# Kernel optimization log

Hardware: AMD Instinct MI355X
Metric: run time of the kernel (lower is better)

Reference implementation:

```python
import jax, jax.numpy as jnp
import numpy as np

B, S, HID = 2, 2048, 1024
NUM_HEADS, HEAD_DIM = 16, 64
GRID_SIZE = 16                 # crop_size // patch_size
ROT_DIM = 2 * (HEAD_DIM // 3 // 2)  # = 20, per axial segment (d, h, w)


def setup_inputs() -> dict:
    key = jax.random.key(0)
    ks = jax.random.split(key, 9)
    sc = 1.0 / np.sqrt(HID)
    return {
        "hidden_states": jax.random.normal(ks[0], (B, S, HID), jnp.float32),
        "Wq": jax.random.normal(ks[1], (HID, HID), jnp.float32) * sc,
        "bq": jax.random.normal(ks[2], (HID,), jnp.float32) * 0.02,
        "Wk": jax.random.normal(ks[3], (HID, HID), jnp.float32) * sc,
        "bk": jax.random.normal(ks[4], (HID,), jnp.float32) * 0.02,
        "Wv": jax.random.normal(ks[5], (HID, HID), jnp.float32) * sc,
        "bv": jax.random.normal(ks[6], (HID,), jnp.float32) * 0.02,
        "Wo": jax.random.normal(ks[7], (HID, HID), jnp.float32) * sc,
        "bo": jax.random.normal(ks[8], (HID,), jnp.float32) * 0.02,
    }


def _rotate(x, pos):
    # x: [B, H, S, D], pos: [S] int. Matches torch rotate_queries_or_keys:
    # sin/cos are TILED (repeat) along the last dim, not interleaved.
    D = x.shape[-1]
    half = D // 2
    omega = 1.0 / (10000.0 ** (jnp.arange(half, dtype=x.dtype) / half))
    freq = pos.astype(x.dtype)[:, None] * omega           # [S, half]
    sin = jnp.tile(jnp.sin(freq), (1, 2))                 # [S, D]
    cos = jnp.tile(jnp.cos(freq), (1, 2))
    y = x.reshape(x.shape[:-1] + (half, 2))
    rot = jnp.stack((-y[..., 1], y[..., 0]), axis=-1).reshape(x.shape)
    return x * cos + rot * sin


def _apply_axial_rope(qk, frame_ids, height_ids, width_ids):
    d = ROT_DIM
    parts = [
        _rotate(qk[..., 0:d], frame_ids),
        _rotate(qk[..., d:2 * d], height_ids),
        _rotate(qk[..., 2 * d:3 * d], width_ids),
    ]
    if 3 * d < qk.shape[-1]:
        parts.append(qk[..., 3 * d:])  # un-rotated tail
    return jnp.concatenate(parts, axis=-1)


def reference(hidden_states, Wq, bq, Wk, bk, Wv, bv, Wo, bo):
    Bq, Sq, _ = hidden_states.shape

    def heads(x):  # [B,S,HID] -> [B,H,S,Dh]
        return x.reshape(Bq, Sq, NUM_HEADS, HEAD_DIM).transpose(0, 2, 1, 3)

    q = heads(hidden_states @ Wq + bq)
    k = heads(hidden_states @ Wk + bk)
    v = heads(hidden_states @ Wv + bv)

    # 3D axial position ids from flat token index
    ids = jnp.arange(Sq)
    tokens_per_frame = GRID_SIZE * GRID_SIZE
    frame_ids = ids // tokens_per_frame
    rem = ids - tokens_per_frame * frame_ids
    height_ids = rem // GRID_SIZE
    width_ids = rem - GRID_SIZE * height_ids

    k = _apply_axial_rope(k, frame_ids, height_ids, width_ids)
    q = _apply_axial_rope(q, frame_ids, height_ids, width_ids)

    scaling = HEAD_DIM ** -0.5
    scores = jnp.einsum("bhqd,bhkd->bhqk", q, k) * scaling
    probs = jax.nn.softmax(scores.astype(jnp.float32), axis=-1).astype(q.dtype)
    ctx = jnp.einsum("bhqk,bhkd->bhqd", probs, v)
    ctx = ctx.transpose(0, 2, 1, 3).reshape(Bq, Sq, HID)
    return ctx @ Wo + bo
```

## Files before the change

kernel.cpp:

```cpp
#include <hip/hip_runtime.h>
#include <hip/hip_bf16.h>

#define B_   2
#define S_   2048
#define HID_ 1024
#define NH_  16
#define HD_  64

typedef __hip_bfloat16 bf16;
typedef __attribute__((ext_vector_type(8))) short s8v;
typedef __attribute__((ext_vector_type(4))) short s4v;
typedef __attribute__((ext_vector_type(4))) float f4v;

#define QSCALE 0.18033688011112042f

__device__ __forceinline__ unsigned short f2b_rne(float x) {
    unsigned int u = __float_as_uint(x);
    u += 0x7fffu + ((u >> 16) & 1u);
    return (unsigned short)(u >> 16);
}

__device__ __forceinline__ void gload_lds16(const void* g, void* l) {
    __builtin_amdgcn_global_load_lds(
        (const __attribute__((address_space(1))) void*)g,
        (__attribute__((address_space(3))) void*)l, 16, 0, 0);
}

__device__ __forceinline__ s4v pack_p(float p0, float p1, float p2, float p3) {
    union { uint2 u; s4v s; } c;
    c.u.x = __builtin_amdgcn_perm(__float_as_uint(p1), __float_as_uint(p0), 0x07060302u);
    c.u.y = __builtin_amdgcn_perm(__float_as_uint(p3), __float_as_uint(p2), 0x07060302u);
    return c.s;
}

__global__ __launch_bounds__(256) void prep_kernel(
    const float* __restrict__ X,
    const float* __restrict__ W0, const float* __restrict__ W1,
    const float* __restrict__ W2, const float* __restrict__ W3,
    unsigned short* __restrict__ Xb,
    unsigned short* __restrict__ T0, unsigned short* __restrict__ T1,
    unsigned short* __restrict__ T2, unsigned short* __restrict__ T3)
{
    const int z = blockIdx.z;
    const int t = threadIdx.x;

    if (z >= 4) {
        const size_t base = ((size_t)(z - 4) * 256 + blockIdx.y * 16 + blockIdx.x) * 4096;
        #pragma unroll
        for (int p = 0; p < 4; ++p) {
            const size_t i = base + p * 1024 + t * 4;
            const float4 f = *reinterpret_cast<const float4*>(X + i);
            ushort4 u;
            u.x = f2b_rne(f.x); u.y = f2b_rne(f.y); u.z = f2b_rne(f.z); u.w = f2b_rne(f.w);
            *reinterpret_cast<ushort4*>(Xb + i) = u;
        }
        return;
    }

    const float* __restrict__ W = (z == 0) ? W0 : (z == 1) ? W1 : (z == 2) ? W2 : W3;
    unsigned short* __restrict__ T = (z == 0) ? T0 : (z == 1) ? T1 : (z == 2) ? T2 : T3;

    __shared__ float Tl[64][65];
    const int n0 = blockIdx.x * 64, k0 = blockIdx.y * 64;
    const int rr = t >> 4, c4 = (t & 15) * 4;

    #pragma unroll
    for (int i = 0; i < 4; ++i) {
        const int kr = i * 16 + rr;
        const float4 f = *reinterpret_cast<const float4*>(W + (size_t)(k0 + kr) * HID_ + n0 + c4);
        Tl[c4 + 0][kr] = f.x; Tl[c4 + 1][kr] = f.y;
        Tl[c4 + 2][kr] = f.z; Tl[c4 + 3][kr] = f.w;
    }
    __syncthreads();
    #pragma unroll
    for (int i = 0; i < 4; ++i) {
        const int nr = i * 16 + rr;
        ushort4 u;
        u.x = f2b_rne(Tl[nr][c4 + 0]); u.y = f2b_rne(Tl[nr][c4 + 1]);
        u.z = f2b_rne(Tl[nr][c4 + 2]); u.w = f2b_rne(Tl[nr][c4 + 3]);
        *reinterpret_cast<ushort4*>(T + (size_t)(n0 + nr) * HID_ + k0 + c4) = u;
    }
}

__device__ __forceinline__ void gemm_stage(
    const unsigned short* __restrict__ Ag, const unsigned short* __restrict__ Bg,
    unsigned short* As, unsigned short* Bs,
    int m0, int n0, int k0, int w, int srow, int lc8)
{
    #pragma unroll
    for (int it = 0; it < 4; ++it) {
        const int row = it * 32 + srow;
        const int sb = (it * 256 + w * 64) * 8;
        gload_lds16(Ag + (size_t)(m0 + row) * HID_ + k0 + lc8, As + sb);
        gload_lds16(Bg + (size_t)(n0 + row) * HID_ + k0 + lc8, Bs + sb);
    }
}

__device__ __forceinline__ void mfma_mainloop_db(
    const unsigned short* __restrict__ Ag, const unsigned short* __restrict__ Bg,
    unsigned short (*As)[128 * 64], unsigned short (*Bs)[128 * 64],
    int m0, int n0, int t, f4v acc[4][4])
{
    const int w = t >> 6, lane = t & 63;
    const int l15 = lane & 15, qd = lane >> 4;
    const int wm = (w & 1) * 64, wn = (w >> 1) * 64;
    const int srow = w * 8 + (lane >> 3);
    const int lc8  = (((lane & 7) ^ (lane >> 3)) * 8);

    gemm_stage(Ag, Bg, As[0], Bs[0], m0, n0, 0, w, srow, lc8);

    for (int kt = 0; kt < HID_ / 64; ++kt) {
        __builtin_amdgcn_s_waitcnt(0x0f70);
        __builtin_amdgcn_s_barrier();
        if (kt < HID_ / 64 - 1)
            gemm_stage(Ag, Bg, As[(kt + 1) & 1], Bs[(kt + 1) & 1],
                       m0, n0, (kt + 1) * 64, w, srow, lc8);

        const unsigned short* Acur = As[kt & 1];
        const unsigned short* Bcur = Bs[kt & 1];
        #pragma unroll
        for (int kc = 0; kc < 2; ++kc) {
            const int p = ((kc * 4 + qd) ^ (l15 & 7)) * 8;
            s8v af[4], bf[4];
            #pragma unroll
            for (int mt = 0; mt < 4; ++mt)
                af[mt] = *reinterpret_cast<const s8v*>(Acur + (wm + mt * 16 + l15) * 64 + p);
            #pragma unroll
            for (int nt = 0; nt < 4; ++nt)
                bf[nt] = *reinterpret_cast<const s8v*>(Bcur + (wn + nt * 16 + l15) * 64 + p);
            #pragma unroll
            for (int mt = 0; mt < 4; ++mt)
                #pragma unroll
                for (int nt = 0; nt < 4; ++nt)
                    acc[mt][nt] = __builtin_amdgcn_mfma_f32_16x16x32_bf16(
                        af[mt], bf[nt], acc[mt][nt], 0, 0, 0);
        }
    }
}

__global__ __launch_bounds__(256, 2) void gemm_qkv_kernel(
    const unsigned short* __restrict__ Xb, const unsigned short* __restrict__ Wt,
    const float* __restrict__ bq, const float* __restrict__ bk, const float* __restrict__ bv,
    unsigned short* __restrict__ Qb, unsigned short* __restrict__ Kb,
    unsigned short* __restrict__ Vt)
{
    const int n0g = blockIdx.x * 128;
    const int z   = n0g >> 10;
    const int n0  = n0g & 1023;
    const int m0  = blockIdx.y * 128;
    const float* __restrict__ bias = (z == 0) ? bq : (z == 1) ? bk : bv;

    const int t = threadIdx.x;
    const int w = t >> 6, lane = t & 63;
    const int l15 = lane & 15, qd = lane >> 4;
    const int wm = (w & 1) * 64, wn = (w >> 1) * 64;

    __shared__ unsigned short As[2][128 * 64];
    __shared__ unsigned short Bs[2][128 * 64];

    f4v acc[4][4];
    #pragma unroll
    for (int mt = 0; mt < 4; ++mt)
        #pragma unroll
        for (int nt = 0; nt < 4; ++nt) acc[mt][nt] = (f4v){0.f, 0.f, 0.f, 0.f};

    mfma_mainloop_db(Xb, Wt, As, Bs, m0, n0g, t, acc);

    const float osc = (z == 0) ? QSCALE : 1.f;

    #pragma unroll
    for (int nt = 0; nt < 4; ++nt) {
        const int col = n0 + wn + nt * 16 + l15;
        const int h = col >> 6, d = col & 63;
        const float bsc = bias[col];
        const int seg = d / 20;
        const int ds  = d - seg * 20;
        const float om   = __expf(-0.9210340372f * (float)(ds % 10));
        const float sign = (d & 1) ? 1.f : -1.f;

        #pragma unroll
        for (int mt = 0; mt < 4; ++mt) {
            const int mbase = m0 + wm + mt * 16 + qd * 4;
            const int b = mbase >> 11;
            const int sbase = mbase & 2047;
            if (z == 2) {
                ushort4 u;
                unsigned short* up = (unsigned short*)&u;
                #pragma unroll
                for (int r = 0; r < 4; ++r) up[r] = f2b_rne(acc[mt][nt][r] + bsc);
                *reinterpret_cast<ushort4*>(
                    Vt + ((size_t)(b * NH_ + h) * HD_ + d) * S_ + sbase) = u;
            } else {
                unsigned short* __restrict__ dst = (z == 0 ? Qb : Kb)
                    + ((size_t)(b * NH_ + h) * S_ + sbase) * HD_ + d;
                #pragma unroll
                for (int r = 0; r < 4; ++r) {
                    const int s = sbase + r;
                    float v = acc[mt][nt][r] + bsc;
                    const float xp = __shfl_xor(v, 1);
                    if (d < 60) {
                        const int rem = s & 255;
                        const float pos = (float)(seg == 0 ? (s >> 8)
                                               : (seg == 1 ? (rem >> 4) : (rem & 15)));
                        const float a = pos * om;
                        float sn, cs;
                        __sincosf(a, &sn, &cs);
                        v = v * cs + sign * xp * sn;
                    }
                    dst[(size_t)r * HD_] = f2b_rne(v * osc);
                }
            }
        }
    }
}

__global__ __launch_bounds__(256, 2) void gemm_out_kernel(
    const unsigned short* __restrict__ Cb, const unsigned short* __restrict__ Wot,
    const float* __restrict__ bo, float* __restrict__ out)
{
    const int n0 = blockIdx.x * 128, m0 = blockIdx.y * 128;
    const int t = threadIdx.x;
    const int w = t >> 6, lane = t & 63;
    const int l15 = lane & 15, qd = lane >> 4;
    const int wm = (w & 1) * 64, wn = (w >> 1) * 64;

    __shared__ unsigned short As[2][128 * 64];
    __shared__ unsigned short Bs[2][128 * 64];

    f4v acc[4][4];
    #pragma unroll
    for (int mt = 0; mt < 4; ++mt)
        #pragma unroll
        for (int nt = 0; nt < 4; ++nt) acc[mt][nt] = (f4v){0.f, 0.f, 0.f, 0.f};

    mfma_mainloop_db(Cb, Wot, As, Bs, m0, n0, t, acc);

    #pragma unroll
    for (int nt = 0; nt < 4; ++nt) {
        const int col = n0 + wn + nt * 16 + l15;
        const float bsc = bo[col];
        #pragma unroll
        for (int mt = 0; mt < 4; ++mt) {
            const int mbase = m0 + wm + mt * 16 + qd * 4;
            #pragma unroll
            for (int r = 0; r < 4; ++r)
                out[(size_t)(mbase + r) * HID_ + col] = acc[mt][nt][r] + bsc;
        }
    }
}

__global__ __launch_bounds__(256, 2) void attn_kernel(
    const bf16* __restrict__ Qb, const bf16* __restrict__ Kb,
    const bf16* __restrict__ Vt, unsigned short* __restrict__ Cb)
{
    const int q0 = blockIdx.x * 128;
    const int bh = blockIdx.y;
    const int b  = bh >> 4, h = bh & 15;
    const int t  = threadIdx.x;
    const int w  = t >> 6;
    const int lane = t & 63;
    const int l15 = lane & 15, qd = lane >> 4;

    __shared__ unsigned short Ks[2][128 * 64];
    __shared__ unsigned short Vs[2][64 * 128];

    s8v bq[2][2];
    #pragma unroll
    for (int g = 0; g < 2; ++g) {
        const bf16* Qrow = Qb + ((size_t)bh * S_ + q0 + w * 32 + g * 16 + l15) * HD_ + qd * 8;
        bq[g][0] = *reinterpret_cast<const s8v*>(Qrow);
        bq[g][1] = *reinterpret_cast<const s8v*>(Qrow + 32);
    }

    f4v oacc[2][4];
    f4v lones[2];
    #pragma unroll
    for (int g = 0; g < 2; ++g) {
        lones[g] = (f4v){0.f, 0.f, 0.f, 0.f};
        #pragma unroll
        for (int dt = 0; dt < 4; ++dt) oacc[g][dt] = (f4v){0.f, 0.f, 0.f, 0.f};
    }

    s4v vone;
    { union { uint2 u; s4v s; } c; c.u = make_uint2(0x3F803F80u, 0x3F803F80u); vone = c.s; }

    const bf16* __restrict__ Kg = Kb + (size_t)bh * S_ * HD_;
    const bf16* __restrict__ Vg = Vt + (size_t)bh * HD_ * S_;

    const int krow = lane >> 3;
    const int ksw  = ((lane & 7) ^ krow) * 8;
    const int vrow = lane >> 4;

    auto stage = [&](int tile, unsigned short* Kd, unsigned short* Vd) {
        const int k0 = tile * 128;
        #pragma unroll
        for (int it = 0; it < 4; ++it) {
            gload_lds16(Kg + (size_t)(k0 + w * 32 + it * 8 + krow) * HD_ + ksw,
                        Kd + (w * 32 + it * 8) * 64);
        }
        #pragma unroll
        for (int it = 0; it < 4; ++it) {
            const int r = w * 16 + it * 4 + vrow;
            const int sv = ((lane & 15) ^ (r & 15)) * 8;
            gload_lds16(Vg + (size_t)r * S_ + k0 + sv,
                        Vd + (w * 16 + it * 4) * 128);
        }
    };

    stage(0, Ks[0], Vs[0]);

    for (int tt = 0; tt < S_ / 128; ++tt) {
        __builtin_amdgcn_s_waitcnt(0x0f70);
        __builtin_amdgcn_s_barrier();
        if (tt < S_ / 128 - 1)
            stage(tt + 1, Ks[(tt + 1) & 1], Vs[(tt + 1) & 1]);

        const unsigned short* K_ = Ks[tt & 1];
        const unsigned short* V_ = Vs[tt & 1];

        #pragma unroll
        for (int nt = 0; nt < 8; ++nt) {
            const unsigned short* kr = K_ + (nt * 16 + l15) * 64;
            const s8v ak0 = *reinterpret_cast<const s8v*>(kr + ((qd ^ (l15 & 7)) * 8));
            const s8v ak1 = *reinterpret_cast<const s8v*>(kr + (((qd + 4) ^ (l15 & 7)) * 8));

            s4v bv[4];
            #pragma unroll
            for (int dt = 0; dt < 4; ++dt) {
                const int r = dt * 16 + l15;
                const int c = nt * 2 + (qd >> 1);
                bv[dt] = *reinterpret_cast<const s4v*>(
                    V_ + r * 128 + ((c ^ l15) & 15) * 8 + (qd & 1) * 4);
            }

            #pragma unroll
            for (int g = 0; g < 2; ++g) {
                f4v zz = (f4v){0.f, 0.f, 0.f, 0.f};
                zz = __builtin_amdgcn_mfma_f32_16x16x32_bf16(ak0, bq[g][0], zz, 0, 0, 0);
                zz = __builtin_amdgcn_mfma_f32_16x16x32_bf16(ak1, bq[g][1], zz, 0, 0, 0);
                const float p0 = __builtin_amdgcn_exp2f(zz[0]);
                const float p1 = __builtin_amdgcn_exp2f(zz[1]);
                const float p2 = __builtin_amdgcn_exp2f(zz[2]);
                const float p3 = __builtin_amdgcn_exp2f(zz[3]);
                const s4v pf = pack_p(p0, p1, p2, p3);
                #pragma unroll
                for (int dt = 0; dt < 4; ++dt)
                    oacc[g][dt] = __builtin_amdgcn_mfma_f32_16x16x16bf16_1k(
                        pf, bv[dt], oacc[g][dt], 0, 0, 0);
                lones[g] = __builtin_amdgcn_mfma_f32_16x16x16bf16_1k(
                    pf, vone, lones[g], 0, 0, 0);
            }
        }
    }

    #pragma unroll
    for (int g = 0; g < 2; ++g) {
        #pragma unroll
        for (int r = 0; r < 4; ++r) {
            const float inv = 1.0f / lones[g][r];
            const int s = q0 + w * 32 + g * 16 + qd * 4 + r;
            unsigned short* __restrict__ dst =
                Cb + ((size_t)(b * S_ + s)) * HID_ + h * HD_ + l15;
            #pragma unroll
            for (int dt = 0; dt < 4; ++dt)
                dst[dt * 16] = f2b_rne(oacc[g][dt][r] * inv);
        }
    }
}

extern "C" void kernel_launch(void* const* d_in, const int* in_sizes, int n_in,
                              void* d_out, int out_size, void* d_ws, size_t ws_size,
                              hipStream_t stream)
{
    const float* X  = (const float*)d_in[0];
    const float* Wq = (const float*)d_in[1];
    const float* bq = (const float*)d_in[2];
    const float* Wk = (const float*)d_in[3];
    const float* bk = (const float*)d_in[4];
    const float* Wv = (const float*)d_in[5];
    const float* bv = (const float*)d_in[6];
    const float* Wo = (const float*)d_in[7];
    const float* bo = (const float*)d_in[8];
    float* out = (float*)d_out;

    const size_t QKV = (size_t)B_ * NH_ * S_ * HD_;
    const size_t WSZ = (size_t)HID_ * HID_;
    unsigned short* Wot = (unsigned short*)d_ws;
    unsigned short* Xb  = Wot + WSZ;
    unsigned short* Wqt = Xb  + QKV;
    unsigned short* Wkt = Wqt + WSZ;
    unsigned short* Wvt = Wkt + WSZ;
    unsigned short* Qb  = Wvt + WSZ;
    unsigned short* Kb  = Qb + QKV;
    unsigned short* Vt  = Kb + QKV;
    unsigned short* Cb  = Vt + QKV;

    prep_kernel<<<dim3(16, 16, 8), 256, 0, stream>>>(
        X, Wq, Wk, Wv, Wo, Xb, Wqt, Wkt, Wvt, Wot);
    gemm_qkv_kernel<<<dim3(24, 32), 256, 0, stream>>>(
        Xb, Wqt, bq, bk, bv, Qb, Kb, Vt);
    attn_kernel<<<dim3(S_ / 128, B_ * NH_), 256, 0, stream>>>(
        (const bf16*)Qb, (const bf16*)Kb, (const bf16*)Vt, Cb);
    gemm_out_kernel<<<dim3(8, 32), 256, 0, stream>>>(Cb, Wot, bo, out);
}
```

Before: 190.5 us.

## Replace ones-MFMA row-sum with VALU accumulation and remap blocks per XCD

The softmax denominator was computed by an extra MFMA against a vector of ones. It is now accumulated with VALU adds on the bf16-rounded probabilities and reduced across lanes with shuffles at the end, which removes one of five MFMAs per inner step. Work-group indices are also remapped so that consecutive blocks landing on the same XCD share the same batch-head, so K/V tiles get reused in that XCD's L2. The cost is extra VALU work and shuffles, and the remap assumes round-robin dispatch across eight XCDs.

```diff
diff --git a/kernel.cpp b/kernel.cpp
--- a/kernel.cpp
+++ b/kernel.cpp
@@ -24,13 +24,6 @@
     __builtin_amdgcn_global_load_lds(
         (const __attribute__((address_space(1))) void*)g,
         (__attribute__((address_space(3))) void*)l, 16, 0, 0);
-}
-
-__device__ __forceinline__ s4v pack_p(float p0, float p1, float p2, float p3) {
-    union { uint2 u; s4v s; } c;
-    c.u.x = __builtin_amdgcn_perm(__float_as_uint(p1), __float_as_uint(p0), 0x07060302u);
-    c.u.y = __builtin_amdgcn_perm(__float_as_uint(p3), __float_as_uint(p2), 0x07060302u);
-    return c.s;
 }
 
 __global__ __launch_bounds__(256) void prep_kernel(
@@ -253,8 +246,11 @@
     const bf16* __restrict__ Qb, const bf16* __restrict__ Kb,
     const bf16* __restrict__ Vt, unsigned short* __restrict__ Cb)
 {
-    const int q0 = blockIdx.x * 128;
-    const int bh = blockIdx.y;
+    const int flat = blockIdx.y * 16 + blockIdx.x;
+    const int xcd  = flat & 7;
+    const int slot = flat >> 3;
+    const int bh   = xcd * 4 + (slot >> 4);
+    const int q0   = (slot & 15) * 128;
     const int b  = bh >> 4, h = bh & 15;
     const int t  = threadIdx.x;
     const int w  = t >> 6;
@@ -273,16 +269,11 @@
     }
 
     f4v oacc[2][4];
-    f4v lones[2];
-    #pragma unroll
-    for (int g = 0; g < 2; ++g) {
-        lones[g] = (f4v){0.f, 0.f, 0.f, 0.f};
+    float lacc[2] = {0.f, 0.f};
+    #pragma unroll
+    for (int g = 0; g < 2; ++g)
         #pragma unroll
         for (int dt = 0; dt < 4; ++dt) oacc[g][dt] = (f4v){0.f, 0.f, 0.f, 0.f};
-    }
-
-    s4v vone;
-    { union { uint2 u; s4v s; } c; c.u = make_uint2(0x3F803F80u, 0x3F803F80u); vone = c.s; }
 
     const bf16* __restrict__ Kg = Kb + (size_t)bh * S_ * HD_;
     const bf16* __restrict__ Vg = Vt + (size_t)bh * HD_ * S_;
@@ -342,22 +333,34 @@
                 const float p1 = __builtin_amdgcn_exp2f(zz[1]);
                 const float p2 = __builtin_amdgcn_exp2f(zz[2]);
                 const float p3 = __builtin_amdgcn_exp2f(zz[3]);
-                const s4v pf = pack_p(p0, p1, p2, p3);
+                const unsigned int u01 = __builtin_amdgcn_perm(
+                    __float_as_uint(p1), __float_as_uint(p0), 0x07060302u);
+                const unsigned int u23 = __builtin_amdgcn_perm(
+                    __float_as_uint(p3), __float_as_uint(p2), 0x07060302u);
+                lacc[g] += __uint_as_float(u01 << 16)
+                         + __uint_as_float(u01 & 0xffff0000u)
+                         + __uint_as_float(u23 << 16)
+                         + __uint_as_float(u23 & 0xffff0000u);
+                union { uint2 u; s4v s; } c;
+                c.u = make_uint2(u01, u23);
+                const s4v pf = c.s;
                 #pragma unroll
                 for (int dt = 0; dt < 4; ++dt)
                     oacc[g][dt] = __builtin_amdgcn_mfma_f32_16x16x16bf16_1k(
                         pf, bv[dt], oacc[g][dt], 0, 0, 0);
-                lones[g] = __builtin_amdgcn_mfma_f32_16x16x16bf16_1k(
-                    pf, vone, lones[g], 0, 0, 0);
             }
         }
     }
 
     #pragma unroll
     for (int g = 0; g < 2; ++g) {
+        float ls = lacc[g];
+        ls += __shfl_xor(ls, 16);
+        ls += __shfl_xor(ls, 32);
         #pragma unroll
         for (int r = 0; r < 4; ++r) {
-            const float inv = 1.0f / lones[g][r];
+            const float lr = __shfl(ls, qd * 4 + r);
+            const float inv = 1.0f / lr;
             const int s = q0 + w * 32 + g * 16 + qd * 4 + r;
             unsigned short* __restrict__ dst =
                 Cb + ((size_t)(b * S_ + s)) * HID_ + h * HD_ + l15;
```

Measured after the change: 192.6 us. No clear change (+1.1%).
